# Kernel tuning notes

Measured on AMD Instinct MI355X. Metric: run time of the kernel, lower is better.

Reference implementation:

```python
import jax, jax.numpy as jnp
import numpy as np

IGNORE = 255
KA = 10.0
ITERS = 10
BETA = 0.8


def _l2(x, axis):
    # F.normalize(p=2): divide by max(norm, eps)
    return x / jnp.maximum(jnp.linalg.norm(x, axis=axis, keepdims=True), 1e-12)


def setup_inputs() -> dict:
    key = jax.random.key(0)
    k1, k2, k3, k4 = jax.random.split(key, 4)
    B, K, P, C = 8, 19, 16384, 256
    return {
        "logit": jax.random.normal(k1, (B, K, P), jnp.float32),
        "target": jax.random.randint(k2, (B, P), 0, K, jnp.int32),
        "feat": jax.random.normal(k3, (B, C, P), jnp.float32),
        "epoch": 60,
        "prototypes_dataset": _l2(jax.random.normal(k4, (C, K), jnp.float32), 0),
    }


def reference(logit, target, feat, epoch, prototypes_dataset):
    B, K, P = logit.shape
    C = feat.shape[1]
    dt = feat.dtype

    # scatter-sum per-class prototypes over all (b, p) positions; ignore bucket = K
    index = jnp.where(target == IGNORE, K, target).reshape(-1)            # [B*P]
    feat_flat = jnp.swapaxes(feat, 1, 2).reshape(B * P, C)                # [B*P, C]
    proto = jax.ops.segment_sum(feat_flat, index, num_segments=K + 1)    # [K+1, C]
    counts = jax.ops.segment_sum(jnp.ones_like(index), index, num_segments=K + 1)
    prototypes_sum = proto[:K].T                                          # [C, K]
    counts_batch = counts[:K]                                             # [K]

    # epoch is a static python int; epoch >= start_epoch(51) -> full vMF branch
    feat_norm = _l2(feat, 1)                                              # [B, C, P]
    u_init = _l2(prototypes_sum / (counts_batch.astype(dt) + 1e-6), 0)    # [C, K]
    mask0 = counts_batch == 0
    u = _l2(jnp.where(mask0[None, :], prototypes_dataset, u_init), 0)     # 'part' init
    a = jnp.full((1, 1, K), 1.0 / K, dt)

    dis = jnp.einsum('bcp,ck->bpk', feat_norm, u)                         # [B, P, K]
    e = a * jnp.exp(KA * dis)
    p = e / jnp.sum(e, -1, keepdims=True)
    for _ in range(ITERS):
        # 'avmf': second assignment in torch overwrites -> mean over batch, [1, P, K]
        a = jnp.mean(p, 0, keepdims=True)
        # 'uvmf': new prototypes from soft assignments
        u = _l2(jnp.mean(jnp.einsum('bcp,bpk->bck', feat_norm, p), 0), 0)
        dis = jnp.einsum('bcp,ck->bpk', feat_norm, u)
        e = a * jnp.exp(KA * dis)
        p = e / jnp.sum(e, -1, keepdims=True)

    # vMF_hard_loss computed in torch but 'hard' not in loss_type -> not added
    vmf_loss = jnp.mean(-p * (jnp.log(a + 1e-6) + KA * dis)) / float(np.log(K))
    consist_loss = jnp.mean(-jnp.swapaxes(p, 1, 2) * jax.nn.log_softmax(logit, axis=1))

    # contrast: off-diagonal prototype similarity over classes present in batch
    m = (~mask0).astype(dt)
    gram = u_init.T @ u_init                                              # [K, K]
    Kn = jnp.sum(m)
    contrast_loss = (jnp.sum(gram * (m[:, None] * m[None, :])) - Kn) / (Kn * (Kn - 1))

    # 'tce': truncated CE, clamp per-pixel loss at -log(beta)
    logp = jax.nn.log_softmax(logit, axis=1)                              # [B, K, P]
    safe_t = jnp.where(target == IGNORE, 0, target)
    ce = -jnp.take_along_axis(logp, safe_t[:, None, :], axis=1)[:, 0, :]  # [B, P]
    valid = (target != IGNORE).astype(dt)
    loss = jnp.sum(jnp.maximum(ce, -float(np.log(BETA))) * valid) / (jnp.sum(valid) + 1e-6)

    loss = loss + vmf_loss + contrast_loss + consist_loss
    return (loss, jax.lax.stop_gradient(prototypes_sum), jax.lax.stop_gradient(counts_batch))
```

## Files before the change

### kernel.cpp

```cpp
#include <hip/hip_runtime.h>
#include <hip/hip_bf16.h>
#include <math.h>

#define BB 8
#define KK 19
#define PP 16384
#define CC 256
#define NN (BB*PP)
#define KA_C 10.0f
#define IGNORE_L 255
#define CETHR 0.22314355131420976f
#define ASTRIDE 311296

#define OFF_FEATN   0
#define OFF_FEATNT  16777216
#define OFF_PROTO   33554432
#define OFF_COUNTS  (OFF_PROTO+4864)
#define OFF_SCAL    (OFF_COUNTS+32)
#define OFF_UINIT   (OFF_SCAL+16)
#define OFF_U       (OFF_UINIT+4864)
#define OFF_A       (OFF_U+4864)
#define OFF_UPART   (OFF_A+2490368)
#define OFF_R1      (OFF_UPART+4980736)
#define OFF_NORM    (OFF_R1+77824)

typedef __attribute__((ext_vector_type(8))) short short8v;
typedef __attribute__((ext_vector_type(4))) float f32x4;

static __device__ __forceinline__ float bflo(unsigned int v){
    union{unsigned int i; float f;} x; x.i = v << 16; return x.f;
}
static __device__ __forceinline__ unsigned short f2bf(float f){
    union{float f; unsigned int i;} x; x.f = f;
    unsigned int r = (x.i + 0x7fffu + ((x.i >> 16) & 1u)) >> 16;
    return (unsigned short)r;
}
static __device__ __forceinline__ float rowsum16(float v){
    v += __shfl_xor(v,1); v += __shfl_xor(v,2);
    v += __shfl_xor(v,4); v += __shfl_xor(v,8);
    return v;
}

__global__ __launch_bounds__(256) void counts_kernel(const int* __restrict__ target,
                                                     float* __restrict__ ws) {
    __shared__ int cnt[KK];
    if (threadIdx.x < KK) cnt[threadIdx.x]=0;
    __syncthreads();
    for (int i = blockIdx.x*256 + threadIdx.x; i < NN; i += gridDim.x*256) {
        int t = target[i];
        if (t >= 0 && t < KK) atomicAdd(&cnt[t], 1);
    }
    __syncthreads();
    if (threadIdx.x < KK) atomicAdd(&ws[OFF_COUNTS + threadIdx.x], (float)cnt[threadIdx.x]);
}

__global__ __launch_bounds__(256) void ssct_kernel(const float* __restrict__ feat,
                                                   unsigned short* __restrict__ featn,
                                                   unsigned short* __restrict__ featn_T,
                                                   float* __restrict__ normf) {
    __shared__ float part[4][128];
    __shared__ float rn_lds[128];
    __shared__ unsigned int tTu[128][33];
    int blk = blockIdx.x;
    int b = blk >> 7;
    int px0 = (blk & 127) * 128;
    int tid = threadIdx.x;
    int lane = tid & 63, w = tid >> 6;
    int pxl = px0 + lane*2;
    const float* fb = feat + (size_t)b*CC*PP;
    float a0=0.f, a1=0.f;
    for (int cc=0; cc<64; cc+=8) {
        float2 v[8];
#pragma unroll
        for (int j=0;j<8;j++) v[j] = *(const float2*)&fb[(size_t)(w*64+cc+j)*PP + pxl];
#pragma unroll
        for (int j=0;j<8;j++) { a0 = fmaf(v[j].x,v[j].x,a0); a1 = fmaf(v[j].y,v[j].y,a1); }
    }
    part[w][lane*2]   = a0;
    part[w][lane*2+1] = a1;
    __syncthreads();
    if (tid < 128) {
        float ss = part[0][tid]+part[1][tid]+part[2][tid]+part[3][tid];
        float nrm = fmaxf(sqrtf(ss), 1e-12f);
        normf[(size_t)b*PP + px0 + tid] = nrm;
        rn_lds[tid] = 1.0f/nrm;
    }
    __syncthreads();
    float rv0 = rn_lds[lane*2], rv1 = rn_lds[lane*2+1];
    unsigned short* ob  = featn + (size_t)b*CC*PP;
    unsigned short* obT = featn_T + ((size_t)b*PP + px0)*CC;
    for (int sl=0; sl<4; sl++) {
        int c0s = sl*64;
#pragma unroll
        for (int jj=0; jj<16; jj+=2) {
            int cl = w*16 + jj;
            int c = c0s + cl;
            float2 va = *(const float2*)&fb[(size_t)c*PP + pxl];
            float2 vb = *(const float2*)&fb[(size_t)(c+1)*PP + pxl];
            unsigned int loA = f2bf(va.x*rv0), hiA = f2bf(va.y*rv1);
            unsigned int loB = f2bf(vb.x*rv0), hiB = f2bf(vb.y*rv1);
            *(unsigned int*)&ob[(size_t)c*PP + pxl]     = (hiA<<16)|loA;
            *(unsigned int*)&ob[(size_t)(c+1)*PP + pxl] = (hiB<<16)|loB;
            tTu[lane*2][cl>>1]   = loA | (loB<<16);
            tTu[lane*2+1][cl>>1] = hiA | (hiB<<16);
        }
        __syncthreads();
#pragma unroll
        for (int j=0; j<16; j++) {
            int flat = j*256 + tid;
            int px = flat >> 5, cu = flat & 31;
            *(unsigned int*)&obT[(size_t)px*CC + c0s + cu*2] = tTu[px][cu];
        }
        __syncthreads();
    }
}

__global__ __launch_bounds__(256) void proto_mfma_kernel(const unsigned short* __restrict__ featn,
                                                         const int* __restrict__ target,
                                                         const float* __restrict__ normf,
                                                         float* __restrict__ upart) {
    __shared__ int tgt_lds[4][64];
    __shared__ unsigned short nrm_lds[4][64];
    int tid = threadIdx.x;
    int blk = blockIdx.x;
    int pxtile = blk & 255;
    int bgrp = blk >> 8;
    {
        int bi = tid >> 6, j = tid & 63;
        int bb = bgrp*4 + bi;
        tgt_lds[bi][j] = target[(size_t)bb*PP + pxtile*64 + j];
        nrm_lds[bi][j] = f2bf(normf[(size_t)bb*PP + pxtile*64 + j]);
    }
    __syncthreads();
    int lane = tid & 63, wid = tid >> 6;
    int g = lane >> 4, lc = lane & 15;

    f32x4 upacc[4][2];
#pragma unroll
    for (int m=0;m<4;m++)
#pragma unroll
        for (int n=0;n<2;n++) upacc[m][n] = (f32x4){0.f,0.f,0.f,0.f};

    for (int bi=0; bi<4; bi++) {
        int bb = bgrp*4 + bi;
        union { unsigned int u[4]; short8v s; } bfr[2][2];
#pragma unroll
        for (int ks=0; ks<2; ks++) {
            int pxo = ks*32 + g*8;
#pragma unroll
            for (int j2=0;j2<4;j2++) {
                int p0i = pxo + 2*j2, p1i = pxo + 2*j2 + 1;
                int t0 = tgt_lds[bi][p0i], t1 = tgt_lds[bi][p1i];
                unsigned int n0 = nrm_lds[bi][p0i], n1 = nrm_lds[bi][p1i];
                int kk1 = lc + 16;
                bfr[ks][0].u[j2] = (t0==lc ? n0:0u) | ((t1==lc ? n1:0u)<<16);
                bfr[ks][1].u[j2] = (t0==kk1? n0:0u) | ((t1==kk1? n1:0u)<<16);
            }
        }
#pragma unroll
        for (int m=0;m<4;m++) {
            int c = wid*64 + m*16 + lc;
            const unsigned short* fr = featn + ((size_t)bb*CC + c)*PP + pxtile*64;
#pragma unroll
            for (int ks=0; ks<2; ks++) {
                int pxo = ks*32 + g*8;
                union { uint4 u4; short8v s; } af2;
                af2.u4 = *(const uint4*)&fr[pxo];
                upacc[m][0] = __builtin_amdgcn_mfma_f32_16x16x32_bf16(af2.s, bfr[ks][0].s, upacc[m][0], 0,0,0);
                upacc[m][1] = __builtin_amdgcn_mfma_f32_16x16x32_bf16(af2.s, bfr[ks][1].s, upacc[m][1], 0,0,0);
            }
        }
    }
#pragma unroll
    for (int m=0;m<4;m++) {
        int cb = wid*64 + m*16 + g*4;
#pragma unroll
        for (int n=0;n<2;n++) {
            int kk = lc + 16*n;
            if (kk < KK) {
#pragma unroll
                for (int r=0;r<4;r++)
                    upart[(size_t)blk*4864 + (size_t)(cb+r)*KK + kk] = upacc[m][n][r];
            }
        }
    }
}

__global__ __launch_bounds__(256) void setup_kernel(const float* __restrict__ pd,
                                                    float* __restrict__ ws) {
    int c = threadIdx.x;
    __shared__ float red[256];
    __shared__ float nrm[KK];
    __shared__ float lds_ui[256][KK];
    float cnts[KK], vi[KK];
#pragma unroll
    for (int k=0;k<KK;k++) cnts[k] = ws[OFF_COUNTS+k];
#pragma unroll
    for (int k=0;k<KK;k++) vi[k] = ws[OFF_PROTO + c*KK + k] / (cnts[k] + 1e-6f);
    for (int k=0;k<KK;k++) {
        red[c] = vi[k]*vi[k];
        __syncthreads();
        for (int s=128;s>0;s>>=1){ if (c<s) red[c]+=red[c+s]; __syncthreads(); }
        if (c==0) nrm[k] = fmaxf(sqrtf(red[0]), 1e-12f);
        __syncthreads();
    }
#pragma unroll
    for (int k=0;k<KK;k++) { vi[k] = vi[k]/nrm[k]; lds_ui[c][k] = vi[k]; ws[OFF_UINIT + c*KK + k] = vi[k]; }
    __syncthreads();
    float w0[KK];
#pragma unroll
    for (int k=0;k<KK;k++) w0[k] = (cnts[k]==0.f) ? pd[c*KK+k] : vi[k];
    for (int k=0;k<KK;k++) {
        red[c] = w0[k]*w0[k];
        __syncthreads();
        for (int s=128;s>0;s>>=1){ if (c<s) red[c]+=red[c+s]; __syncthreads(); }
        if (c==0) nrm[k] = fmaxf(sqrtf(red[0]), 1e-12f);
        __syncthreads();
    }
#pragma unroll
    for (int k=0;k<KK;k++) ws[OFF_U + k*CC + c] = w0[k] / nrm[k];
    float m[KK]; float Kn=0.f;
#pragma unroll
    for (int k=0;k<KK;k++){ m[k] = (cnts[k]==0.f)?0.f:1.f; Kn += m[k]; }
    float csum = 0.f;
    for (int idx = c; idx < KK*KK; idx += 256) {
        int k1 = idx / KK, k2 = idx % KK;
        if (m[k1]!=0.f && m[k2]!=0.f) {
            float gg=0.f;
            for (int cc2=0; cc2<CC; cc2++) gg += lds_ui[cc2][k1]*lds_ui[cc2][k2];
            csum += gg;
        }
    }
    red[c]=csum; __syncthreads();
    for (int s=128;s>0;s>>=1){ if (c<s) red[c]+=red[c+s]; __syncthreads(); }
    if (c==0) ws[OFF_SCAL+4] = (red[0] - Kn) / (Kn * (Kn - 1.f));
}

__global__ __launch_bounds__(256) void pu_kernel(const unsigned short* __restrict__ featn,
                                                 const unsigned short* __restrict__ featn_T,
                                                 const float* __restrict__ ubuf,
                                                 const float* __restrict__ aRbase,
                                                 float* __restrict__ aWbase,
                                                 float* __restrict__ upart,
                                                 int uniform_a) {
    __shared__ __attribute__((aligned(16))) unsigned short u_lds[32*264];
    __shared__ __attribute__((aligned(16))) unsigned short p_lds[32*72];
    int tid = threadIdx.x;
    for (int i=tid; i<32*256; i+=256) {
        int k = i>>8, c = i&255;
        u_lds[k*264+c] = (k<KK) ? f2bf(ubuf[k*CC+c]) : (unsigned short)0;
    }
    __syncthreads();
    int blk = blockIdx.x;
    int pxtile = blk & 255;
    int bgrp = blk >> 8;
    int lane = tid & 63, wid = tid >> 6;
    int g = lane >> 4, lc = lane & 15;
    int px_w = pxtile*64 + wid*16;

    float a0r[4], a1r[4];
    if (uniform_a) {
#pragma unroll
        for (int r=0;r<4;r++){ a0r[r]=1.0f/(float)KK; a1r[r]=1.0f/(float)KK; }
    } else {
        int k1 = (lc+16 > KK-1) ? (KK-1) : (lc+16);
#pragma unroll
        for (int r=0;r<4;r++) {
            int pxg = px_w + g*4 + r;
            float s0 = aRbase[0*ASTRIDE + (size_t)lc*PP+pxg] + aRbase[1*ASTRIDE + (size_t)lc*PP+pxg]
                     + aRbase[2*ASTRIDE + (size_t)lc*PP+pxg] + aRbase[3*ASTRIDE + (size_t)lc*PP+pxg];
            float s1 = aRbase[0*ASTRIDE + (size_t)k1*PP+pxg] + aRbase[1*ASTRIDE + (size_t)k1*PP+pxg]
                     + aRbase[2*ASTRIDE + (size_t)k1*PP+pxg] + aRbase[3*ASTRIDE + (size_t)k1*PP+pxg];
            a0r[r] = s0*0.125f;
            a1r[r] = s1*0.125f;
        }
    }

    f32x4 upacc[4][2];
#pragma unroll
    for (int m=0;m<4;m++)
#pragma unroll
        for (int n=0;n<2;n++) upacc[m][n] = (f32x4){0.f,0.f,0.f,0.f};
    float aacc[2][4];
#pragma unroll
    for (int n=0;n<2;n++)
#pragma unroll
        for (int r=0;r<4;r++) aacc[n][r]=0.f;

    for (int bi=0; bi<2; bi++) {
        int bb = bgrp*2 + bi;
        const unsigned short* fb = featn + (size_t)bb*CC*PP;
        const unsigned short* fTrow = featn_T + ((size_t)bb*PP + px_w + lc)*CC;
        f32x4 acc0 = (f32x4){0.f,0.f,0.f,0.f};
        f32x4 acc1 = (f32x4){0.f,0.f,0.f,0.f};
#pragma unroll
        for (int ks=0; ks<8; ks++) {
            int cbase = ks*32 + g*8;
            union { uint4 u4; short8v s; } af, bf0, bf1;
            af.u4  = *(const uint4*)&fTrow[cbase];
            bf0.u4 = *(const uint4*)&u_lds[(size_t)lc*264 + cbase];
            bf1.u4 = *(const uint4*)&u_lds[(size_t)(lc+16)*264 + cbase];
            acc0 = __builtin_amdgcn_mfma_f32_16x16x32_bf16(af.s, bf0.s, acc0, 0,0,0);
            acc1 = __builtin_amdgcn_mfma_f32_16x16x32_bf16(af.s, bf1.s, acc1, 0,0,0);
        }
#pragma unroll
        for (int r=0;r<4;r++) {
            float e0 = a0r[r] * __expf(KA_C * acc0[r]);
            float e1 = (lc+16 < KK) ? a1r[r] * __expf(KA_C * acc1[r]) : 0.f;
            float sv = rowsum16(e0 + e1);
            float inv = 1.0f/sv;
            float p0 = e0*inv, p1 = e1*inv;
            aacc[0][r] += p0; aacc[1][r] += p1;
            int pl = wid*16 + g*4 + r;
            p_lds[(size_t)lc*72 + pl]      = f2bf(p0);
            p_lds[(size_t)(lc+16)*72 + pl] = f2bf(p1);
        }
        __syncthreads();
#pragma unroll
        for (int m=0;m<4;m++) {
            int c = wid*64 + m*16 + lc;
            const unsigned short* fr = fb + (size_t)c*PP + pxtile*64;
#pragma unroll
            for (int ks=0; ks<2; ks++) {
                int pxo = ks*32 + g*8;
                union { uint4 u4; short8v s; } af2, bp0, bp1;
                af2.u4 = *(const uint4*)&fr[pxo];
                bp0.u4 = *(const uint4*)&p_lds[(size_t)lc*72 + pxo];
                bp1.u4 = *(const uint4*)&p_lds[(size_t)(lc+16)*72 + pxo];
                upacc[m][0] = __builtin_amdgcn_mfma_f32_16x16x32_bf16(af2.s, bp0.s, upacc[m][0], 0,0,0);
                upacc[m][1] = __builtin_amdgcn_mfma_f32_16x16x32_bf16(af2.s, bp1.s, upacc[m][1], 0,0,0);
            }
        }
        __syncthreads();
    }
#pragma unroll
    for (int m=0;m<4;m++) {
        int cb = wid*64 + m*16 + g*4;
#pragma unroll
        for (int n=0;n<2;n++) {
            int kk = lc + 16*n;
            if (kk < KK) {
#pragma unroll
                for (int r=0;r<4;r++)
                    upart[(size_t)blk*4864 + (size_t)(cb+r)*KK + kk] = upacc[m][n][r];
            }
        }
    }
    float* aOut = aWbase + (size_t)bgrp*ASTRIDE;
#pragma unroll
    for (int n=0;n<2;n++) {
        int kk = lc + 16*n;
        if (kk < KK) {
#pragma unroll
            for (int r=0;r<4;r++) {
                int pxg = px_w + g*4 + r;
                aOut[(size_t)kk*PP + pxg] = aacc[n][r];
            }
        }
    }
}

__global__ __launch_bounds__(256) void r1_kernel(const float* __restrict__ upart,
                                                 float* __restrict__ r1buf) {
    int blk = blockIdx.x;
    int echunk = blk % 19;
    int ichunk = blk / 19;
    int e = echunk*256 + threadIdx.x;
    float s = 0.f;
    int i0 = ichunk*64;
    for (int i=i0; i<i0+64; i++) s += upart[(size_t)i*4864 + e];
    r1buf[(size_t)ichunk*4864 + e] = s;
}

__global__ __launch_bounds__(256) void r2_kernel(const float* __restrict__ r1buf,
                                                 float* __restrict__ ws, int nbuf) {
    int k = blockIdx.x;
    int c = threadIdx.x;
    float s = 0.f;
    for (int i=0;i<nbuf;i++) s += r1buf[(size_t)i*4864 + c*KK + k];
    __shared__ float red[256];
    red[c] = s*s; __syncthreads();
    for (int q=128;q>0;q>>=1){ if (c<q) red[c]+=red[c+q]; __syncthreads(); }
    float nrm = fmaxf(sqrtf(red[0]), 1e-12f);
    ws[OFF_U + k*CC + c] = s / nrm;
}

__global__ __launch_bounds__(256) void protored2_kernel(const float* __restrict__ r1buf,
                                                        float* __restrict__ ws, int nbuf) {
    int e = blockIdx.x*256 + threadIdx.x;
    float s = 0.f;
    for (int i=0;i<nbuf;i++) s += r1buf[(size_t)i*4864 + e];
    ws[OFF_PROTO + e] = s;
}

__global__ __launch_bounds__(256) void final_kernel(const unsigned short* __restrict__ featn,
                                                    const float* __restrict__ logit,
                                                    const int* __restrict__ target,
                                                    const float* __restrict__ ws_u,
                                                    const float* __restrict__ aFbase,
                                                    float* __restrict__ scal) {
    __shared__ float lu[4864];
    for (int i=threadIdx.x; i<4864; i+=256) lu[i] = ws_u[i];
    __syncthreads();
    int n = blockIdx.x*256 + threadIdx.x;
    int b = n >> 14;
    int pix = n & (PP-1);
    const unsigned short* fcol = featn + (size_t)b*CC*PP + pix;
    float dot[KK];
#pragma unroll
    for (int k=0;k<KK;k++) dot[k]=0.f;
    for (int c0=0; c0<CC; c0+=16) {
        float fv[16];
#pragma unroll
        for (int j=0;j<16;j++) {
            unsigned int u16 = fcol[(size_t)(c0+j)*PP];
            fv[j] = bflo(u16);
        }
#pragma unroll
        for (int k=0;k<KK;k++) {
            float d = dot[k];
#pragma unroll
            for (int j=0;j<16;j++) d = fmaf(fv[j], lu[k*CC+c0+j], d);
            dot[k]=d;
        }
    }
    float e[KK]; float den=0.f; float av[KK];
#pragma unroll
    for (int k=0;k<KK;k++) {
        av[k] = (aFbase[0*ASTRIDE + (size_t)k*PP + pix] + aFbase[1*ASTRIDE + (size_t)k*PP + pix]
               + aFbase[2*ASTRIDE + (size_t)k*PP + pix] + aFbase[3*ASTRIDE + (size_t)k*PP + pix])*0.125f;
        e[k] = av[k] * __expf(KA_C * dot[k]);
        den += e[k];
    }
    float inv = 1.0f/den;
    float vmf = 0.f;
#pragma unroll
    for (int k=0;k<KK;k++) {
        vmf += -(e[k]*inv) * (__logf(av[k] + 1e-6f) + KA_C * dot[k]);
    }
    float lg[KK]; float mx = -3.4e38f;
#pragma unroll
    for (int k=0;k<KK;k++) { lg[k] = logit[((size_t)b*KK + k)*PP + pix]; mx = fmaxf(mx, lg[k]); }
    float sme = 0.f;
#pragma unroll
    for (int k=0;k<KK;k++) sme += __expf(lg[k]-mx);
    float lse = mx + __logf(sme);
    float cons = 0.f;
#pragma unroll
    for (int k=0;k<KK;k++) cons += -(e[k]*inv) * (lg[k]-lse);
    int t = target[(size_t)b*PP + pix];
    float ce_n = 0.f, ce_d = 0.f;
    if (t != IGNORE_L) {
        float lt = 0.f;
#pragma unroll
        for (int k=0;k<KK;k++) lt = (t==k) ? lg[k] : lt;
        float ce = -(lt - lse);
        ce_n = fmaxf(ce, CETHR);
        ce_d = 1.f;
    }
    __shared__ float red[4][4];
    int lane = threadIdx.x & 63, w = threadIdx.x >> 6;
    float v0=vmf, v1=cons, v2=ce_n, v3=ce_d;
#pragma unroll
    for (int s=32;s>0;s>>=1) {
        v0 += __shfl_xor(v0, s); v1 += __shfl_xor(v1, s);
        v2 += __shfl_xor(v2, s); v3 += __shfl_xor(v3, s);
    }
    if (lane==0){ red[w][0]=v0; red[w][1]=v1; red[w][2]=v2; red[w][3]=v3; }
    __syncthreads();
    if (threadIdx.x==0) {
        atomicAdd(&scal[0], red[0][0]+red[1][0]+red[2][0]+red[3][0]);
        atomicAdd(&scal[1], red[0][1]+red[1][1]+red[2][1]+red[3][1]);
        atomicAdd(&scal[2], red[0][2]+red[1][2]+red[2][2]+red[3][2]);
        atomicAdd(&scal[3], red[0][3]+red[1][3]+red[2][3]+red[3][3]);
    }
}

__global__ __launch_bounds__(256) void finalize_kernel(const float* __restrict__ ws,
                                                       float* __restrict__ out) {
    if (blockIdx.x==0 && threadIdx.x==0) {
        float cnt_all = (float)BB*(float)PP*(float)KK;
        float vmf  = ws[OFF_SCAL+0] / cnt_all / logf((float)KK);
        float cons = ws[OFF_SCAL+1] / cnt_all;
        float ce   = ws[OFF_SCAL+2] / (ws[OFF_SCAL+3] + 1e-6f);
        float contrast = ws[OFF_SCAL+4];
        out[0] = ce + vmf + contrast + cons;
    }
    int i = blockIdx.x*256 + threadIdx.x;
    if (i < 4864) out[1+i] = ws[OFF_PROTO+i];
    if (blockIdx.x==0 && threadIdx.x < KK) out[1+4864+threadIdx.x] = ws[OFF_COUNTS+threadIdx.x];
}

extern "C" void kernel_launch(void* const* d_in, const int* in_sizes, int n_in,
                              void* d_out, int out_size, void* d_ws, size_t ws_size,
                              hipStream_t stream) {
    (void)in_sizes; (void)n_in; (void)out_size; (void)ws_size;
    const float* logit  = (const float*)d_in[0];
    const int*   target = (const int*)d_in[1];
    const float* feat   = (const float*)d_in[2];
    const float* pd     = (const float*)d_in[4];
    float* out = (float*)d_out;
    float* ws  = (float*)d_ws;

    unsigned short* featn   = (unsigned short*)ws;
    unsigned short* featn_T = (unsigned short*)(ws + OFF_FEATNT);
    float* ubuf  = ws + OFF_U;
    float* upart = ws + OFF_UPART;
    float* r1buf = ws + OFF_R1;
    float* normf = ws + OFF_NORM;
    float* scal  = ws + OFF_SCAL;
    float* aSet[2] = { ws + OFF_A, ws + OFF_A + (size_t)4*ASTRIDE };

    hipMemsetAsync(ws + OFF_PROTO, 0, 4912*sizeof(float), stream);
    ssct_kernel<<<1024, 256, 0, stream>>>(feat, featn, featn_T, normf);
    counts_kernel<<<256, 256, 0, stream>>>(target, ws);
    proto_mfma_kernel<<<512, 256, 0, stream>>>(featn, target, normf, upart);
    r1_kernel<<<152, 256, 0, stream>>>(upart, r1buf);
    protored2_kernel<<<19, 256, 0, stream>>>(r1buf, ws, 8);
    setup_kernel<<<1, 256, 0, stream>>>(pd, ws);

    for (int t=0; t<10; t++) {
        if (t > 0) {
            r1_kernel<<<304, 256, 0, stream>>>(upart, r1buf);
            r2_kernel<<<KK, 256, 0, stream>>>(r1buf, ws, 16);
        }
        pu_kernel<<<1024, 256, 0, stream>>>(featn, featn_T, ubuf,
                                            aSet[t&1], aSet[(t+1)&1],
                                            upart, (t==0)?1:0);
    }
    r1_kernel<<<304, 256, 0, stream>>>(upart, r1buf);
    r2_kernel<<<KK, 256, 0, stream>>>(r1buf, ws, 16);
    final_kernel<<<512, 256, 0, stream>>>(featn, logit, target, ubuf, aSet[0], scal);
    finalize_kernel<<<20, 256, 0, stream>>>(ws, out);
}
```

Baseline: 674.3 us.

## Store assignment buffer pixel-major, precompute bf16 prototypes, retile normalization kernel

Measured after the change: 617.0 us. 1.09x faster.

```diff
diff --git a/kernel.cpp b/kernel.cpp
--- a/kernel.cpp
+++ b/kernel.cpp
@@ -10,7 +10,7 @@
 #define KA_C 10.0f
 #define IGNORE_L 255
 #define CETHR 0.22314355131420976f
-#define ASTRIDE 311296
+#define AQ 524288
 
 #define OFF_FEATN   0
 #define OFF_FEATNT  16777216
@@ -19,8 +19,9 @@
 #define OFF_SCAL    (OFF_COUNTS+32)
 #define OFF_UINIT   (OFF_SCAL+16)
 #define OFF_U       (OFF_UINIT+4864)
-#define OFF_A       (OFF_U+4864)
-#define OFF_UPART   (OFF_A+2490368)
+#define OFF_UBF     (OFF_U+4864)
+#define OFF_A       (OFF_UBF+4224)
+#define OFF_UPART   (OFF_A+8*AQ)
 #define OFF_R1      (OFF_UPART+4980736)
 #define OFF_NORM    (OFF_R1+77824)
 
@@ -58,60 +59,46 @@
                                                    unsigned short* __restrict__ featn,
                                                    unsigned short* __restrict__ featn_T,
                                                    float* __restrict__ normf) {
-    __shared__ float part[4][128];
-    __shared__ float rn_lds[128];
-    __shared__ unsigned int tTu[128][33];
+    __shared__ float part[4][64];
+    __shared__ float rn_lds[64];
+    __shared__ unsigned short tTus[64][270];
     int blk = blockIdx.x;
-    int b = blk >> 7;
-    int px0 = (blk & 127) * 128;
+    int b = blk >> 8;
+    int px0 = (blk & 255) * 64;
     int tid = threadIdx.x;
-    int lane = tid & 63, w = tid >> 6;
-    int pxl = px0 + lane*2;
+    int l = tid & 63, w = tid >> 6;
     const float* fb = feat + (size_t)b*CC*PP;
-    float a0=0.f, a1=0.f;
-    for (int cc=0; cc<64; cc+=8) {
-        float2 v[8];
-#pragma unroll
-        for (int j=0;j<8;j++) v[j] = *(const float2*)&fb[(size_t)(w*64+cc+j)*PP + pxl];
-#pragma unroll
-        for (int j=0;j<8;j++) { a0 = fmaf(v[j].x,v[j].x,a0); a1 = fmaf(v[j].y,v[j].y,a1); }
-    }
-    part[w][lane*2]   = a0;
-    part[w][lane*2+1] = a1;
-    __syncthreads();
-    if (tid < 128) {
-        float ss = part[0][tid]+part[1][tid]+part[2][tid]+part[3][tid];
-        float nrm = fmaxf(sqrtf(ss), 1e-12f);
+    int c0 = w*64;
+    float ss = 0.f;
+    for (int cc=0; cc<64; cc++) {
+        float v = fb[(size_t)(c0+cc)*PP + px0 + l];
+        ss = fmaf(v, v, ss);
+    }
+    part[w][l] = ss;
+    __syncthreads();
+    if (tid < 64) {
+        float s = part[0][tid]+part[1][tid]+part[2][tid]+part[3][tid];
+        float nrm = fmaxf(sqrtf(s), 1e-12f);
         normf[(size_t)b*PP + px0 + tid] = nrm;
         rn_lds[tid] = 1.0f/nrm;
     }
     __syncthreads();
-    float rv0 = rn_lds[lane*2], rv1 = rn_lds[lane*2+1];
-    unsigned short* ob  = featn + (size_t)b*CC*PP;
+    float r = rn_lds[l];
+    unsigned short* ob  = featn + (size_t)b*CC*PP + px0;
+    for (int cc=0; cc<64; cc++) {
+        int c = c0 + cc;
+        float v = fb[(size_t)c*PP + px0 + l];
+        unsigned short us = f2bf(v * r);
+        ob[(size_t)c*PP + l] = us;
+        tTus[l][c] = us;
+    }
+    __syncthreads();
     unsigned short* obT = featn_T + ((size_t)b*PP + px0)*CC;
-    for (int sl=0; sl<4; sl++) {
-        int c0s = sl*64;
-#pragma unroll
-        for (int jj=0; jj<16; jj+=2) {
-            int cl = w*16 + jj;
-            int c = c0s + cl;
-            float2 va = *(const float2*)&fb[(size_t)c*PP + pxl];
-            float2 vb = *(const float2*)&fb[(size_t)(c+1)*PP + pxl];
-            unsigned int loA = f2bf(va.x*rv0), hiA = f2bf(va.y*rv1);
-            unsigned int loB = f2bf(vb.x*rv0), hiB = f2bf(vb.y*rv1);
-            *(unsigned int*)&ob[(size_t)c*PP + pxl]     = (hiA<<16)|loA;
-            *(unsigned int*)&ob[(size_t)(c+1)*PP + pxl] = (hiB<<16)|loB;
-            tTu[lane*2][cl>>1]   = loA | (loB<<16);
-            tTu[lane*2+1][cl>>1] = hiA | (hiB<<16);
-        }
-        __syncthreads();
-#pragma unroll
-        for (int j=0; j<16; j++) {
-            int flat = j*256 + tid;
-            int px = flat >> 5, cu = flat & 31;
-            *(unsigned int*)&obT[(size_t)px*CC + c0s + cu*2] = tTu[px][cu];
-        }
-        __syncthreads();
+    for (int j=0; j<32; j++) {
+        int flat = j*256 + tid;
+        int px = flat >> 7, cu = flat & 127;
+        unsigned int v = *(const unsigned int*)&tTus[px][cu*2];
+        *(unsigned int*)&obT[(size_t)px*CC + cu*2] = v;
     }
 }
 
@@ -217,8 +204,13 @@
         if (c==0) nrm[k] = fmaxf(sqrtf(red[0]), 1e-12f);
         __syncthreads();
     }
-#pragma unroll
-    for (int k=0;k<KK;k++) ws[OFF_U + k*CC + c] = w0[k] / nrm[k];
+    unsigned short* ubf = (unsigned short*)(ws + OFF_UBF);
+#pragma unroll
+    for (int k=0;k<KK;k++) {
+        float uv = w0[k] / nrm[k];
+        ws[OFF_U + k*CC + c] = uv;
+        ubf[k*264 + c] = f2bf(uv);
+    }
     float m[KK]; float Kn=0.f;
 #pragma unroll
     for (int k=0;k<KK;k++){ m[k] = (cnts[k]==0.f)?0.f:1.f; Kn += m[k]; }
@@ -238,7 +230,7 @@
 
 __global__ __launch_bounds__(256) void pu_kernel(const unsigned short* __restrict__ featn,
                                                  const unsigned short* __restrict__ featn_T,
-                                                 const float* __restrict__ ubuf,
+                                                 const unsigned short* __restrict__ ubf,
                                                  const float* __restrict__ aRbase,
                                                  float* __restrict__ aWbase,
                                                  float* __restrict__ upart,
@@ -246,9 +238,10 @@
     __shared__ __attribute__((aligned(16))) unsigned short u_lds[32*264];
     __shared__ __attribute__((aligned(16))) unsigned short p_lds[32*72];
     int tid = threadIdx.x;
-    for (int i=tid; i<32*256; i+=256) {
-        int k = i>>8, c = i&255;
-        u_lds[k*264+c] = (k<KK) ? f2bf(ubuf[k*CC+c]) : (unsigned short)0;
+    {
+        const uint4* src = (const uint4*)ubf;
+        uint4* dst = (uint4*)u_lds;
+        for (int i=tid; i<1056; i+=256) dst[i] = src[i];
     }
     __syncthreads();
     int blk = blockIdx.x;
@@ -267,10 +260,10 @@
 #pragma unroll
         for (int r=0;r<4;r++) {
             int pxg = px_w + g*4 + r;
-            float s0 = aRbase[0*ASTRIDE + (size_t)lc*PP+pxg] + aRbase[1*ASTRIDE + (size_t)lc*PP+pxg]
-                     + aRbase[2*ASTRIDE + (size_t)lc*PP+pxg] + aRbase[3*ASTRIDE + (size_t)lc*PP+pxg];
-            float s1 = aRbase[0*ASTRIDE + (size_t)k1*PP+pxg] + aRbase[1*ASTRIDE + (size_t)k1*PP+pxg]
-                     + aRbase[2*ASTRIDE + (size_t)k1*PP+pxg] + aRbase[3*ASTRIDE + (size_t)k1*PP+pxg];
+            float s0 = aRbase[0*AQ + (size_t)pxg*32 + lc] + aRbase[1*AQ + (size_t)pxg*32 + lc]
+                     + aRbase[2*AQ + (size_t)pxg*32 + lc] + aRbase[3*AQ + (size_t)pxg*32 + lc];
+            float s1 = aRbase[0*AQ + (size_t)pxg*32 + k1] + aRbase[1*AQ + (size_t)pxg*32 + k1]
+                     + aRbase[2*AQ + (size_t)pxg*32 + k1] + aRbase[3*AQ + (size_t)pxg*32 + k1];
             a0r[r] = s0*0.125f;
             a1r[r] = s1*0.125f;
         }
@@ -346,7 +339,7 @@
             }
         }
     }
-    float* aOut = aWbase + (size_t)bgrp*ASTRIDE;
+    float* aOut = aWbase + (size_t)bgrp*AQ;
 #pragma unroll
     for (int n=0;n<2;n++) {
         int kk = lc + 16*n;
@@ -354,7 +347,7 @@
 #pragma unroll
             for (int r=0;r<4;r++) {
                 int pxg = px_w + g*4 + r;
-                aOut[(size_t)kk*PP + pxg] = aacc[n][r];
+                aOut[(size_t)pxg*32 + kk] = aacc[n][r];
             }
         }
     }
@@ -382,7 +375,9 @@
     red[c] = s*s; __syncthreads();
     for (int q=128;q>0;q>>=1){ if (c<q) red[c]+=red[c+q]; __syncthreads(); }
     float nrm = fmaxf(sqrtf(red[0]), 1e-12f);
-    ws[OFF_U + k*CC + c] = s / nrm;
+    float uv = s / nrm;
+    ws[OFF_U + k*CC + c] = uv;
+    ((unsigned short*)(ws + OFF_UBF))[k*264 + c] = f2bf(uv);
 }
 
 __global__ __launch_bounds__(256) void protored2_kernel(const float* __restrict__ r1buf,
@@ -427,8 +422,8 @@
     float e[KK]; float den=0.f; float av[KK];
 #pragma unroll
     for (int k=0;k<KK;k++) {
-        av[k] = (aFbase[0*ASTRIDE + (size_t)k*PP + pix] + aFbase[1*ASTRIDE + (size_t)k*PP + pix]
-               + aFbase[2*ASTRIDE + (size_t)k*PP + pix] + aFbase[3*ASTRIDE + (size_t)k*PP + pix])*0.125f;
+        av[k] = (aFbase[0*AQ + (size_t)pix*32 + k] + aFbase[1*AQ + (size_t)pix*32 + k]
+               + aFbase[2*AQ + (size_t)pix*32 + k] + aFbase[3*AQ + (size_t)pix*32 + k])*0.125f;
         e[k] = av[k] * __expf(KA_C * dot[k]);
         den += e[k];
     }
@@ -504,15 +499,17 @@
 
     unsigned short* featn   = (unsigned short*)ws;
     unsigned short* featn_T = (unsigned short*)(ws + OFF_FEATNT);
+    unsigned short* ubf     = (unsigned short*)(ws + OFF_UBF);
     float* ubuf  = ws + OFF_U;
     float* upart = ws + OFF_UPART;
     float* r1buf = ws + OFF_R1;
     float* normf = ws + OFF_NORM;
     float* scal  = ws + OFF_SCAL;
-    float* aSet[2] = { ws + OFF_A, ws + OFF_A + (size_t)4*ASTRIDE };
+    float* aSet[2] = { ws + OFF_A, ws + OFF_A + (size_t)4*AQ };
 
     hipMemsetAsync(ws + OFF_PROTO, 0, 4912*sizeof(float), stream);
-    ssct_kernel<<<1024, 256, 0, stream>>>(feat, featn, featn_T, normf);
+    hipMemsetAsync(ws + OFF_UBF, 0, 4224*sizeof(float), stream);
+    ssct_kernel<<<2048, 256, 0, stream>>>(feat, featn, featn_T, normf);
     counts_kernel<<<256, 256, 0, stream>>>(target, ws);
     proto_mfma_kernel<<<512, 256, 0, stream>>>(featn, target, normf, upart);
     r1_kernel<<<152, 256, 0, stream>>>(upart, r1buf);
@@ -524,7 +521,7 @@
             r1_kernel<<<304, 256, 0, stream>>>(upart, r1buf);
             r2_kernel<<<KK, 256, 0, stream>>>(r1buf, ws, 16);
         }
-        pu_kernel<<<1024, 256, 0, stream>>>(featn, featn_T, ubuf,
+        pu_kernel<<<1024, 256, 0, stream>>>(featn, featn_T, ubf,
                                             aSet[t&1], aSet[(t+1)&1],
                                             upart, (t==0)?1:0);
     }
```
